# Kernel optimization log

Hardware: AMD Instinct MI355X
Metric: run time of the kernel (lower is better)

Reference implementation:

```python
import jax, jax.numpy as jnp
import numpy as np

DIM = 1024
N_HEADS = 16
HEAD_DIM = DIM // N_HEADS
MAX_SEQ = 2048
B, S = 4, 2048


def _rope_tables(seq_len):
    inv_freq = 1.0 / (10000.0 ** (jnp.arange(0, HEAD_DIM, 2, dtype=jnp.float32) / HEAD_DIM))
    t = jnp.arange(seq_len, dtype=jnp.float32)
    freqs = jnp.outer(t, inv_freq)            # [S, HEAD_DIM/2]
    emb = jnp.concatenate([freqs, freqs], -1)  # [S, HEAD_DIM]
    return jnp.cos(emb), jnp.sin(emb)


def _apply_rope(x, cos, sin):
    # x: [B, S, H, Dh]; cos/sin: [S, Dh]
    c = cos[None, :, None, :]
    s = sin[None, :, None, :]
    x1, x2 = jnp.split(x, 2, axis=-1)
    x_rot = jnp.concatenate([-x2, x1], -1)
    return x * c + x_rot * s


def setup_inputs() -> dict:
    key = jax.random.key(0)
    kx, kq, kk, kv, ko = jax.random.split(key, 5)
    std = DIM ** -0.5
    x = jax.random.normal(kx, (B, S, DIM), jnp.float32)
    Wq = jax.random.normal(kq, (DIM, DIM), jnp.float32) * std
    Wk = jax.random.normal(kk, (DIM, DIM), jnp.float32) * std
    Wv = jax.random.normal(kv, (DIM, DIM), jnp.float32) * std
    Wo = jax.random.normal(ko, (DIM, DIM), jnp.float32) * std
    # causal mask: 1 where attending is allowed, 0 where masked (mask==0 -> -inf)
    mask = jnp.tril(jnp.ones((S, S), jnp.int32))[None, None]  # [1,1,S,S]
    return {"x": x, "Wq": Wq, "Wk": Wk, "Wv": Wv, "Wo": Wo, "mask": mask}


def reference(x, Wq, Wk, Wv, Wo, mask) -> jnp.ndarray:
    b, s, _ = x.shape
    scale = HEAD_DIM ** -0.5
    # torch Linear: y = x @ W.T, W is [out, in]
    q = (x @ Wq.T).reshape(b, s, N_HEADS, HEAD_DIM)
    k = (x @ Wk.T).reshape(b, s, N_HEADS, HEAD_DIM)
    v = (x @ Wv.T).reshape(b, s, N_HEADS, HEAD_DIM)
    cos, sin = _rope_tables(s)
    q = _apply_rope(q, cos, sin)
    k = _apply_rope(k, cos, sin)
    # [B, H, S, S]
    attn = jnp.einsum('bqhd,bkhd->bhqk', q, k) * scale
    attn = jnp.where(mask == 0, -jnp.inf, attn)
    attn = jax.nn.softmax(attn, axis=-1)
    out = jnp.einsum('bhqk,bkhd->bqhd', attn, v).reshape(b, s, DIM)
    return out @ Wo.T
```

## Files before the change

kernel.cpp:

```cpp
#include <hip/hip_runtime.h>
#include <hip/hip_bf16.h>
#include <math.h>

using bf16 = __hip_bfloat16;
typedef __attribute__((ext_vector_type(8))) short short8;
typedef __attribute__((ext_vector_type(4))) float float4v;

#define DIM 1024
#define NH 16
#define HD 64
#define BB 4
#define SS 2048
#define MTOT (BB * SS)

#define ROPE_LOG2 0.41524101186092034f
#define PC1 0.18033688f
#define PC0 -23.08312066f

__device__ inline short bf16bits(float x) {
  return __builtin_bit_cast(short, __float2bfloat16(x));
}
__device__ inline float bits2f(unsigned short b) {
  return __builtin_bit_cast(float, (unsigned)b << 16);
}
__device__ inline unsigned pack2(float a, float b) {
  return (unsigned)(unsigned short)bf16bits(a) |
         ((unsigned)(unsigned short)bf16bits(b) << 16);
}

__device__ inline void async16(const void* g, void* l) {
  __builtin_amdgcn_global_load_lds(
      (const __attribute__((address_space(1))) void*)g,
      (__attribute__((address_space(3))) void*)l, 16, 0, 0);
}

__global__ __launch_bounds__(256) void rope_tab_k(unsigned* __restrict__ tab) {
  int i = blockIdx.x * 256 + threadIdx.x;
  int s = i >> 5, d = i & 31;
  float inv = exp2f(-(float)d * ROPE_LOG2);
  float sn, cs;
  sincosf((float)s * inv, &sn, &cs);
  tab[i] = pack2(cs, sn);
}

__device__ inline void cvt8(const float* __restrict__ in, bf16* __restrict__ out,
                            size_t i) {
  const float4v* p = (const float4v*)in + i * 2;
  float4v a = p[0], b = p[1];
  short8 r;
  r[0] = bf16bits(a[0]); r[1] = bf16bits(a[1]);
  r[2] = bf16bits(a[2]); r[3] = bf16bits(a[3]);
  r[4] = bf16bits(b[0]); r[5] = bf16bits(b[1]);
  r[6] = bf16bits(b[2]); r[7] = bf16bits(b[3]);
  ((short8*)out)[i] = r;
}

__global__ __launch_bounds__(256) void cvt_x(const float* __restrict__ in,
                                             bf16* __restrict__ out) {
  cvt8(in, out, (size_t)blockIdx.x * 256 + threadIdx.x);
}

__global__ __launch_bounds__(256) void cvt_w(const float* w0, const float* w1,
                                             const float* w2, const float* w3,
                                             bf16* o0, bf16* o1, bf16* o2,
                                             bf16* o3) {
  const float* in = blockIdx.y == 0 ? w0 : blockIdx.y == 1 ? w1
                    : blockIdx.y == 2 ? w2 : w3;
  bf16* out = blockIdx.y == 0 ? o0 : blockIdx.y == 1 ? o1
              : blockIdx.y == 2 ? o2 : o3;
  cvt8(in, out, (size_t)blockIdx.x * 256 + threadIdx.x);
}

template <int MODE, typename TC>
__global__ __launch_bounds__(256, 2) void gemm_bt(const bf16* __restrict__ A,
                                                  const bf16* __restrict__ W,
                                                  TC* __restrict__ C,
                                                  const unsigned* __restrict__ rt,
                                                  int M, int N, int K) {
  __shared__ __align__(16) short sA[128 * 32];
  __shared__ __align__(16) short sB[128 * 32];
  __shared__ __align__(16) short sT[(MODE == 2) ? 64 * 130 : 1];

  const int tid = threadIdx.x;
  const int wave = tid >> 6;
  const int lane = tid & 63;
  const int l15 = lane & 15;
  const int quad = lane >> 4;
  const int m0 = blockIdx.x * 128;
  const int n0 = blockIdx.y * 128;
  const int wm = (wave >> 1) * 64;
  const int wn = (wave & 1) * 64;

  float4v acc[4][4];
#pragma unroll
  for (int i = 0; i < 4; i++)
#pragma unroll
    for (int j = 0; j < 4; j++)
#pragma unroll
      for (int r = 0; r < 4; r++) acc[i][j][r] = 0.0f;

  for (int k0 = 0; k0 < K; k0 += 32) {
    __syncthreads();
#pragma unroll
    for (int i = 0; i < 2; i++) {
      int c0 = i * 256 + wave * 64;
      int c = c0 + lane;
      int row = c >> 2, cb = c & 3;
      async16(A + (size_t)(m0 + row) * K + k0 + cb * 8, sA + c0 * 8);
      async16(W + (size_t)(n0 + row) * K + k0 + cb * 8, sB + c0 * 8);
    }
    __syncthreads();

    short8 af[4], bfr[4];
#pragma unroll
    for (int mi = 0; mi < 4; mi++)
      af[mi] = *(const short8*)(sA + (wm + mi * 16 + l15) * 32 + quad * 8);
#pragma unroll
    for (int ni = 0; ni < 4; ni++)
      bfr[ni] = *(const short8*)(sB + (wn + ni * 16 + l15) * 32 + quad * 8);
#pragma unroll
    for (int mi = 0; mi < 4; mi++)
#pragma unroll
      for (int ni = 0; ni < 4; ni++)
        acc[mi][ni] = __builtin_amdgcn_mfma_f32_16x16x32_bf16(
            af[mi], bfr[ni], acc[mi][ni], 0, 0, 0);
  }

  if (MODE == 2) {
    const int bb_ = m0 >> 11;
    const int s0 = m0 & (SS - 1);
    const int h0 = n0 >> 6;
#pragma unroll
    for (int half = 0; half < 2; half++) {
      if (half) __syncthreads();
      if ((wave & 1) == half) {
#pragma unroll
        for (int mi = 0; mi < 4; mi++)
#pragma unroll
          for (int ni = 0; ni < 4; ni++)
#pragma unroll
            for (int r = 0; r < 4; r++)
              sT[(ni * 16 + l15) * 130 + wm + mi * 16 + quad * 4 + r] =
                  bf16bits(acc[mi][ni][r]);
      }
      __syncthreads();
      int row = tid >> 2, cb = tid & 3;
      size_t base =
          ((size_t)(bb_ * NH + h0 + half) * HD + row) * SS + s0 + cb * 32;
#pragma unroll
      for (int c = 0; c < 4; c++) {
        short8 vv = *(const short8*)(sT + row * 130 + cb * 32 + c * 8);
        *(short8*)((short*)C + base + c * 8) = vv;
      }
    }
    return;
  }

#pragma unroll
  for (int mi = 0; mi < 4; mi++) {
#pragma unroll
    for (int r = 0; r < 4; r++) {
      int m = m0 + wm + mi * 16 + quad * 4 + r;
      if (MODE == 0) {
#pragma unroll
        for (int ni = 0; ni < 4; ni++) {
          int n = n0 + wn + ni * 16 + l15;
          C[(size_t)m * N + n] = (TC)(acc[mi][ni][r]);
        }
      } else {
        int b = m >> 11;
        int s = m & (SS - 1);
        int h = (n0 + wn) >> 6;
        bf16* outp = (bf16*)C + ((size_t)(b * NH + h) * SS + s) * HD;
#pragma unroll
        for (int ni = 0; ni < 2; ni++) {
          int d = ni * 16 + l15;
          unsigned cspack = rt[s * 32 + d];
          float cs = bits2f((unsigned short)(cspack & 0xffff));
          float sn = bits2f((unsigned short)(cspack >> 16));
          float lo = acc[mi][ni][r];
          float hi = acc[mi][ni + 2][r];
          outp[d] = __float2bfloat16(lo * cs - hi * sn);
          outp[d + 32] = __float2bfloat16(hi * cs + lo * sn);
        }
      }
    }
  }
}

#define SKV 64
#define SP 64

__global__ __launch_bounds__(256, 2) void attn_fwd(const bf16* __restrict__ q,
                                                   const bf16* __restrict__ k,
                                                   const bf16* __restrict__ vt,
                                                   bf16* __restrict__ o) {
  __shared__ __align__(16) short sK[2][64 * SKV];
  __shared__ __align__(16) short sV[2][64 * SKV];
  __shared__ __align__(16) short sP[4][16 * SP];

  const int tid = threadIdx.x;
  const int wave = tid >> 6;
  const int lane = tid & 63;
  const int l15 = lane & 15;
  const int quad = lane >> 4;
  const int bh = blockIdx.x;
  const int p = blockIdx.y;
  const int qt[4] = {p, 15 - p, 16 + p, 31 - p};
  const size_t hb = (size_t)bh * SS * HD;
  const size_t vtb = (size_t)bh * HD * SS;

  short8 aQ[4][2];
#pragma unroll
  for (int ti = 0; ti < 4; ti++) {
    const bf16* qp =
        q + hb + (size_t)(qt[ti] * 64 + wave * 16 + l15) * HD + quad * 8;
    aQ[ti][0] = *(const short8*)qp;
    aQ[ti][1] = *(const short8*)(qp + 32);
  }

  float l_part[4] = {0.0f, 0.0f, 0.0f, 0.0f};
  float4v acc_o[4][4];
#pragma unroll
  for (int ti = 0; ti < 4; ti++)
#pragma unroll
    for (int di = 0; di < 4; di++)
#pragma unroll
      for (int r = 0; r < 4; r++) acc_o[ti][di][r] = 0.0f;

  int4 kr[2], vr[2];
  auto load_kv = [&](int kt_) {
    int k0n = kt_ * 64;
#pragma unroll
    for (int i = 0; i < 2; i++) {
      int c = tid + i * 256;
      kr[i] = *(const int4*)(k + hb + (size_t)(k0n + (c >> 3)) * HD + (c & 7) * 8);
      vr[i] = *(const int4*)(vt + vtb + (size_t)(c >> 3) * SS + k0n + (c & 7) * 8);
    }
  };
  auto stage_write = [&](int buf) {
#pragma unroll
    for (int i = 0; i < 2; i++) {
      int c = tid + i * 256;
      int row = c >> 3;
      int sl = (c & 7) ^ (row & 7);
      *(int4*)(&sK[buf][row * SKV + sl * 8]) = kr[i];
      *(int4*)(&sV[buf][row * SKV + sl * 8]) = vr[i];
    }
  };

  load_kv(0);
  stage_write(0);
  __syncthreads();

  const int maxkt = qt[3];
  for (int kt = 0; kt <= maxkt; kt++) {
    const int cur = kt & 1;
    if (kt < maxkt) load_kv(kt + 1);

    short8 kf[8], vf[8];
#pragma unroll
    for (int t = 0; t < 2; t++)
#pragma unroll
      for (int i = 0; i < 4; i++) {
        int row = i * 16 + l15;
        int sl = (t * 4 + quad) ^ (l15 & 7);
        kf[t * 4 + i] = *(const short8*)(&sK[cur][row * SKV + sl * 8]);
        vf[t * 4 + i] = *(const short8*)(&sV[cur][row * SKV + sl * 8]);
      }

    const int k0 = kt * 64;
    short* pw = &sP[wave][0];
#pragma unroll
    for (int ti = 0; ti < 4; ti++) {
      if (kt <= qt[ti]) {
        float4v s[4];
#pragma unroll
        for (int ni = 0; ni < 4; ni++)
#pragma unroll
          for (int r = 0; r < 4; r++) s[ni][r] = 0.0f;
#pragma unroll
        for (int t = 0; t < 2; t++)
#pragma unroll
          for (int ni = 0; ni < 4; ni++)
            s[ni] = __builtin_amdgcn_mfma_f32_16x16x32_bf16(
                kf[t * 4 + ni], aQ[ti][t], s[ni], 0, 0, 0);

        const bool diag = (kt == qt[ti]);
        const int qglob = qt[ti] * 64 + wave * 16 + l15;
#pragma unroll
        for (int ni = 0; ni < 4; ni++) {
          float pe[4];
#pragma unroll
          for (int r = 0; r < 4; r++) {
            float x = exp2f(fmaf(s[ni][r], PC1, PC0));
            if (diag && (k0 + ni * 16 + quad * 4 + r > qglob)) x = 0.0f;
            l_part[ti] += x;
            pe[r] = x;
          }
          int2 w2;
          w2.x = (int)pack2(pe[0], pe[1]);
          w2.y = (int)pack2(pe[2], pe[3]);
          int slw = (2 * ni + (quad >> 1)) ^ (l15 & 7);
          *(int2*)(pw + l15 * SP + slw * 8 + (quad & 1) * 4) = w2;
        }
        asm volatile("s_waitcnt lgkmcnt(0)" ::: "memory");

#pragma unroll
        for (int t = 0; t < 2; t++) {
          int slr = (t * 4 + quad) ^ (l15 & 7);
          short8 aP = *(const short8*)(pw + l15 * SP + slr * 8);
#pragma unroll
          for (int di = 0; di < 4; di++)
            acc_o[ti][di] = __builtin_amdgcn_mfma_f32_16x16x32_bf16(
                aP, vf[t * 4 + di], acc_o[ti][di], 0, 0, 0);
        }
      }
    }

    if (kt < maxkt) stage_write(cur ^ 1);
    __syncthreads();
  }

  const int b = bh >> 4, h = bh & 15;
#pragma unroll
  for (int ti = 0; ti < 4; ti++) {
    float lr = l_part[ti];
    lr += __shfl_xor(lr, 16, 64);
    lr += __shfl_xor(lr, 32, 64);
#pragma unroll
    for (int r = 0; r < 4; r++) {
      float invl = 1.0f / __shfl(lr, quad * 4 + r, 64);
      bf16* op =
          o + (size_t)(b * SS + qt[ti] * 64 + wave * 16 + quad * 4 + r) * DIM +
          h * HD;
#pragma unroll
      for (int di = 0; di < 4; di++)
        op[di * 16 + l15] = __float2bfloat16(acc_o[ti][di][r] * invl);
    }
  }
}

extern "C" void kernel_launch(void* const* d_in, const int* in_sizes, int n_in,
                              void* d_out, int out_size, void* d_ws,
                              size_t ws_size, hipStream_t stream) {
  const float* x = (const float*)d_in[0];
  const float* Wq = (const float*)d_in[1];
  const float* Wk = (const float*)d_in[2];
  const float* Wv = (const float*)d_in[3];
  const float* Wo = (const float*)d_in[4];
  float* out = (float*)d_out;

  char* ws = (char*)d_ws;
  const size_t xsz = (size_t)MTOT * DIM * sizeof(bf16);
  bf16* xb = (bf16*)ws;
  bf16* qb_ = (bf16*)(ws + xsz);
  bf16* kb = (bf16*)(ws + 2 * xsz);
  bf16* vtb = (bf16*)(ws + 3 * xsz);
  bf16* wqb = (bf16*)(ws + 4 * xsz);
  bf16* wkb = wqb + (size_t)DIM * DIM;
  bf16* wvb = wkb + (size_t)DIM * DIM;
  bf16* wob = wvb + (size_t)DIM * DIM;
  unsigned* rt = (unsigned*)(wob + (size_t)DIM * DIM);
  bf16* ob = xb;

  dim3 bb(256);
  rope_tab_k<<<dim3(SS * 32 / 256), bb, 0, stream>>>(rt);
  cvt_x<<<dim3(MTOT * DIM / 8 / 256), bb, 0, stream>>>(x, xb);
  cvt_w<<<dim3(DIM * DIM / 8 / 256, 4), bb, 0, stream>>>(Wq, Wk, Wv, Wo, wqb,
                                                         wkb, wvb, wob);
  dim3 gg(MTOT / 128, DIM / 128);
  gemm_bt<1, bf16><<<gg, bb, 0, stream>>>(xb, wqb, qb_, rt, MTOT, DIM, DIM);
  gemm_bt<1, bf16><<<gg, bb, 0, stream>>>(xb, wkb, kb, rt, MTOT, DIM, DIM);
  gemm_bt<2, bf16><<<gg, bb, 0, stream>>>(xb, wvb, vtb, rt, MTOT, DIM, DIM);
  attn_fwd<<<dim3(BB * NH, 8), bb, 0, stream>>>(qb_, kb, vtb, ob);
  gemm_bt<0, float><<<gg, bb, 0, stream>>>(ob, wob, out, rt, MTOT, DIM, DIM);
}
```

Before: 321.3 us.

## Fuse Q/K/V projections into one GEMM launch and prioritize MFMA in attention

Merges the three QKV projection GEMMs into a single launch with a 3x wider N grid. It relies on the contiguous layout of wq/wk/wv and of the q/k/vt buffers, and picks the epilogue per block from the N-third. The shared-memory staging buffer now aliases the A/B tiles to cut LDS use. Attention MFMA sections are wrapped in s_setprio to favour matrix issue over other waves. The aim is fewer launches and better tail occupancy, at the cost of divergent epilogue paths inside one kernel.

```diff
diff --git a/kernel.cpp b/kernel.cpp
--- a/kernel.cpp
+++ b/kernel.cpp
@@ -71,15 +71,13 @@
   cvt8(in, out, (size_t)blockIdx.x * 256 + threadIdx.x);
 }
 
-template <int MODE, typename TC>
-__global__ __launch_bounds__(256, 2) void gemm_bt(const bf16* __restrict__ A,
-                                                  const bf16* __restrict__ W,
-                                                  TC* __restrict__ C,
-                                                  const unsigned* __restrict__ rt,
-                                                  int M, int N, int K) {
-  __shared__ __align__(16) short sA[128 * 32];
-  __shared__ __align__(16) short sB[128 * 32];
-  __shared__ __align__(16) short sT[(MODE == 2) ? 64 * 130 : 1];
+__global__ __launch_bounds__(256, 2) void gemm_qkv(
+    const bf16* __restrict__ A, const bf16* __restrict__ W,
+    bf16* __restrict__ Cbase, const unsigned* __restrict__ rt) {
+  __shared__ __align__(16) short sPool[8320];
+  short* sA = sPool;
+  short* sB = sPool + 4096;
+  short* sT = sPool;
 
   const int tid = threadIdx.x;
   const int wave = tid >> 6;
@@ -90,6 +88,7 @@
   const int n0 = blockIdx.y * 128;
   const int wm = (wave >> 1) * 64;
   const int wn = (wave & 1) * 64;
+  const int K = DIM;
 
   float4v acc[4][4];
 #pragma unroll
@@ -126,13 +125,17 @@
             af[mi], bfr[ni], acc[mi][ni], 0, 0, 0);
   }
 
-  if (MODE == 2) {
+  const int third = n0 >> 10;
+  const int nloc = n0 & 1023;
+  bf16* C = Cbase + (size_t)third * MTOT * DIM;
+
+  if (third == 2) {
     const int bb_ = m0 >> 11;
     const int s0 = m0 & (SS - 1);
-    const int h0 = n0 >> 6;
+    const int h0 = nloc >> 6;
 #pragma unroll
     for (int half = 0; half < 2; half++) {
-      if (half) __syncthreads();
+      __syncthreads();
       if ((wave & 1) == half) {
 #pragma unroll
         for (int mi = 0; mi < 4; mi++)
@@ -161,28 +164,86 @@
 #pragma unroll
     for (int r = 0; r < 4; r++) {
       int m = m0 + wm + mi * 16 + quad * 4 + r;
-      if (MODE == 0) {
-#pragma unroll
-        for (int ni = 0; ni < 4; ni++) {
-          int n = n0 + wn + ni * 16 + l15;
-          C[(size_t)m * N + n] = (TC)(acc[mi][ni][r]);
-        }
-      } else {
-        int b = m >> 11;
-        int s = m & (SS - 1);
-        int h = (n0 + wn) >> 6;
-        bf16* outp = (bf16*)C + ((size_t)(b * NH + h) * SS + s) * HD;
-#pragma unroll
-        for (int ni = 0; ni < 2; ni++) {
-          int d = ni * 16 + l15;
-          unsigned cspack = rt[s * 32 + d];
-          float cs = bits2f((unsigned short)(cspack & 0xffff));
-          float sn = bits2f((unsigned short)(cspack >> 16));
-          float lo = acc[mi][ni][r];
-          float hi = acc[mi][ni + 2][r];
-          outp[d] = __float2bfloat16(lo * cs - hi * sn);
-          outp[d + 32] = __float2bfloat16(hi * cs + lo * sn);
-        }
+      int b = m >> 11;
+      int s = m & (SS - 1);
+      int h = (nloc + wn) >> 6;
+      bf16* outp = C + ((size_t)(b * NH + h) * SS + s) * HD;
+#pragma unroll
+      for (int ni = 0; ni < 2; ni++) {
+        int d = ni * 16 + l15;
+        unsigned cspack = rt[s * 32 + d];
+        float cs = bits2f((unsigned short)(cspack & 0xffff));
+        float sn = bits2f((unsigned short)(cspack >> 16));
+        float lo = acc[mi][ni][r];
+        float hi = acc[mi][ni + 2][r];
+        outp[d] = __float2bfloat16(lo * cs - hi * sn);
+        outp[d + 32] = __float2bfloat16(hi * cs + lo * sn);
+      }
+    }
+  }
+}
+
+__global__ __launch_bounds__(256, 2) void gemm_out(const bf16* __restrict__ A,
+                                                   const bf16* __restrict__ W,
+                                                   float* __restrict__ C) {
+  __shared__ __align__(16) short sA[128 * 32];
+  __shared__ __align__(16) short sB[128 * 32];
+
+  const int tid = threadIdx.x;
+  const int wave = tid >> 6;
+  const int lane = tid & 63;
+  const int l15 = lane & 15;
+  const int quad = lane >> 4;
+  const int m0 = blockIdx.x * 128;
+  const int n0 = blockIdx.y * 128;
+  const int wm = (wave >> 1) * 64;
+  const int wn = (wave & 1) * 64;
+  const int K = DIM, N = DIM;
+
+  float4v acc[4][4];
+#pragma unroll
+  for (int i = 0; i < 4; i++)
+#pragma unroll
+    for (int j = 0; j < 4; j++)
+#pragma unroll
+      for (int r = 0; r < 4; r++) acc[i][j][r] = 0.0f;
+
+  for (int k0 = 0; k0 < K; k0 += 32) {
+    __syncthreads();
+#pragma unroll
+    for (int i = 0; i < 2; i++) {
+      int c0 = i * 256 + wave * 64;
+      int c = c0 + lane;
+      int row = c >> 2, cb = c & 3;
+      async16(A + (size_t)(m0 + row) * K + k0 + cb * 8, sA + c0 * 8);
+      async16(W + (size_t)(n0 + row) * K + k0 + cb * 8, sB + c0 * 8);
+    }
+    __syncthreads();
+
+    short8 af[4], bfr[4];
+#pragma unroll
+    for (int mi = 0; mi < 4; mi++)
+      af[mi] = *(const short8*)(sA + (wm + mi * 16 + l15) * 32 + quad * 8);
+#pragma unroll
+    for (int ni = 0; ni < 4; ni++)
+      bfr[ni] = *(const short8*)(sB + (wn + ni * 16 + l15) * 32 + quad * 8);
+#pragma unroll
+    for (int mi = 0; mi < 4; mi++)
+#pragma unroll
+      for (int ni = 0; ni < 4; ni++)
+        acc[mi][ni] = __builtin_amdgcn_mfma_f32_16x16x32_bf16(
+            af[mi], bfr[ni], acc[mi][ni], 0, 0, 0);
+  }
+
+#pragma unroll
+  for (int mi = 0; mi < 4; mi++) {
+#pragma unroll
+    for (int r = 0; r < 4; r++) {
+      int m = m0 + wm + mi * 16 + quad * 4 + r;
+#pragma unroll
+      for (int ni = 0; ni < 4; ni++) {
+        int n = n0 + wn + ni * 16 + l15;
+        C[(size_t)m * N + n] = acc[mi][ni][r];
       }
     }
   }
@@ -279,12 +340,14 @@
         for (int ni = 0; ni < 4; ni++)
 #pragma unroll
           for (int r = 0; r < 4; r++) s[ni][r] = 0.0f;
+        __builtin_amdgcn_s_setprio(1);
 #pragma unroll
         for (int t = 0; t < 2; t++)
 #pragma unroll
           for (int ni = 0; ni < 4; ni++)
             s[ni] = __builtin_amdgcn_mfma_f32_16x16x32_bf16(
                 kf[t * 4 + ni], aQ[ti][t], s[ni], 0, 0, 0);
+        __builtin_amdgcn_s_setprio(0);
 
         const bool diag = (kt == qt[ti]);
         const int qglob = qt[ti] * 64 + wave * 16 + l15;
@@ -306,6 +369,7 @@
         }
         asm volatile("s_waitcnt lgkmcnt(0)" ::: "memory");
 
+        __builtin_amdgcn_s_setprio(1);
 #pragma unroll
         for (int t = 0; t < 2; t++) {
           int slr = (t * 4 + quad) ^ (l15 & 7);
@@ -315,6 +379,7 @@
             acc_o[ti][di] = __builtin_amdgcn_mfma_f32_16x16x32_bf16(
                 aP, vf[t * 4 + di], acc_o[ti][di], 0, 0, 0);
         }
+        __builtin_amdgcn_s_setprio(0);
       }
     }
 
@@ -369,10 +434,8 @@
   cvt_x<<<dim3(MTOT * DIM / 8 / 256), bb, 0, stream>>>(x, xb);
   cvt_w<<<dim3(DIM * DIM / 8 / 256, 4), bb, 0, stream>>>(Wq, Wk, Wv, Wo, wqb,
                                                          wkb, wvb, wob);
-  dim3 gg(MTOT / 128, DIM / 128);
-  gemm_bt<1, bf16><<<gg, bb, 0, stream>>>(xb, wqb, qb_, rt, MTOT, DIM, DIM);
-  gemm_bt<1, bf16><<<gg, bb, 0, stream>>>(xb, wkb, kb, rt, MTOT, DIM, DIM);
-  gemm_bt<2, bf16><<<gg, bb, 0, stream>>>(xb, wvb, vtb, rt, MTOT, DIM, DIM);
+  gemm_qkv<<<dim3(MTOT / 128, 3 * DIM / 128), bb, 0, stream>>>(xb, wqb, qb_,
+                                                               rt);
   attn_fwd<<<dim3(BB * NH, 8), bb, 0, stream>>>(qb_, kb, vtb, ob);
-  gemm_bt<0, float><<<gg, bb, 0, stream>>>(ob, wob, out, rt, MTOT, DIM, DIM);
-}
+  gemm_out<<<dim3(MTOT / 128, DIM / 128), bb, 0, stream>>>(ob, wob, out);
+}
```

Result: faster. 301.4 us (-6.2%).
